# Kernel tuning notes

Hardware: AMD Instinct MI355X
Metric: run time of the kernel (lower is better)

The kernel has to match this reference:

```python
import jax, jax.numpy as jnp
import numpy as np

B, L, D, H = 2, 2048, 1024, 16
P = D // H  # head dim = 64


def setup_inputs() -> dict:
    key = jax.random.key(0)
    ks = jax.random.split(key, 9)
    s = 1.0 / np.sqrt(D)
    x = jax.random.normal(ks[0], (B, L, D), dtype=jnp.float32)
    Wq = jax.random.normal(ks[1], (D, D), dtype=jnp.float32) * s
    bq = jax.random.normal(ks[2], (D,), dtype=jnp.float32) * 0.02
    Wk = jax.random.normal(ks[3], (D, D), dtype=jnp.float32) * s
    bk = jax.random.normal(ks[4], (D,), dtype=jnp.float32) * 0.02
    Wv = jax.random.normal(ks[5], (D, D), dtype=jnp.float32) * s
    bv = jax.random.normal(ks[6], (D,), dtype=jnp.float32) * 0.02
    Wo = jax.random.normal(ks[7], (D, D), dtype=jnp.float32) * s
    bo = jax.random.normal(ks[8], (D,), dtype=jnp.float32) * 0.02
    return {"token_activations": x, "Wq": Wq, "bq": bq, "Wk": Wk, "bk": bk,
            "Wv": Wv, "bv": bv, "Wo": Wo, "bo": bo}


def _split_heads(t):
    # 'b l (h p) -> b h l p'
    b, l, d = t.shape
    return t.reshape(b, l, H, P).transpose(0, 2, 1, 3)


def reference(token_activations, Wq, bq, Wk, bk, Wv, bv, Wo, bo):
    x = token_activations
    q = _split_heads(x @ Wq.T + bq)  # [B,H,L,P]
    k = _split_heads(x @ Wk.T + bk)
    v = _split_heads(x @ Wv.T + bv)
    # pattern[b,h,l,m] = K_l . Q_m / sqrt(P)
    scores = jnp.einsum('bhlp,bhmp->bhlm', k, q) / jnp.sqrt(jnp.float32(P))
    attn = jax.nn.softmax(scores, axis=-2)  # softmax over key axis l
    # out at query position m: sum_l attn[l,m] * V_l
    o = jnp.einsum('bhlm,bhlp->bhmp', attn, v)  # [B,H,L,P] (m indexed)
    o = o.transpose(0, 2, 1, 3).reshape(x.shape[0], x.shape[1], D)  # 'b h m p -> b m (h p)'
    return o @ Wo.T + bo
```

## Files before the change

### kernel.cpp

```cpp
#include <hip/hip_runtime.h>

typedef unsigned short u16;
typedef float f32x4 __attribute__((ext_vector_type(4)));
typedef __bf16 bf16x8 __attribute__((ext_vector_type(8)));
typedef __bf16 bf16x4 __attribute__((ext_vector_type(4)));

#define DEV static __device__ __forceinline__

constexpr int kB = 2;
constexpr int kL = 2048;
constexpr int kD = 1024;
constexpr int kH = 16;
constexpr int kP = 64;
constexpr int kM = kB * kL;
constexpr float kQScale = 0.125f * 1.44269504088896f;

DEV u16 f2bf(float x) {
  union { float f; unsigned u; } v;
  v.f = x;
  unsigned r = v.u + 0x7fffu + ((v.u >> 16) & 1u);
  return (u16)(r >> 16);
}

DEV void gload16(const void* g, void* l) {
  __builtin_amdgcn_global_load_lds(
      (const __attribute__((address_space(1))) unsigned int*)g,
      (__attribute__((address_space(3))) unsigned int*)l, 16, 0, 0);
}

__global__ void cvt_kernel(const float* __restrict__ src, u16* __restrict__ dst, int n4) {
  int i = blockIdx.x * blockDim.x + threadIdx.x;
  if (i >= n4) return;
  float4 v = reinterpret_cast<const float4*>(src)[i];
  uint2 o;
  o.x = (unsigned)f2bf(v.x) | ((unsigned)f2bf(v.y) << 16);
  o.y = (unsigned)f2bf(v.z) | ((unsigned)f2bf(v.w) << 16);
  reinterpret_cast<uint2*>(dst)[i] = o;
}

__global__ void cvtw_kernel(const float* __restrict__ w0, const float* __restrict__ w1,
                            const float* __restrict__ w2, const float* __restrict__ w3,
                            u16* __restrict__ o0, u16* __restrict__ o1,
                            u16* __restrict__ o2, u16* __restrict__ o3) {
  int sel = blockIdx.x >> 10;
  int i = (blockIdx.x & 1023) * 256 + threadIdx.x;
  const float* src = sel == 0 ? w0 : (sel == 1 ? w1 : (sel == 2 ? w2 : w3));
  u16* dst = sel == 0 ? o0 : (sel == 1 ? o1 : (sel == 2 ? o2 : o3));
  float4 v = reinterpret_cast<const float4*>(src)[i];
  uint2 o;
  o.x = (unsigned)f2bf(v.x) | ((unsigned)f2bf(v.y) << 16);
  o.y = (unsigned)f2bf(v.z) | ((unsigned)f2bf(v.w) << 16);
  reinterpret_cast<uint2*>(dst)[i] = o;
}

DEV void gemm_tile(const u16* __restrict__ A, const u16* __restrict__ W,
                   int m0, int n0, u16* As, u16* Bs, f32x4 acc[4][4]) {
  const int tid = threadIdx.x;
  const int w = tid >> 6, lane = tid & 63;
  const int wr = w >> 1, wc = w & 1;
  const int g = lane >> 4, c = lane & 15;
  const int srow = lane >> 2;
  const int skoff = (lane & 3) * 8;

  for (int k0 = 0; k0 < kD; k0 += 32) {
    __syncthreads();
#pragma unroll
    for (int j = 0; j < 2; ++j) {
      const u16* ga = A + (size_t)(m0 + w * 32 + j * 16 + srow) * kD + k0 + skoff;
      gload16(ga, As + (w * 32 + j * 16) * 32);
      const u16* gb = W + (size_t)(n0 + w * 32 + j * 16 + srow) * kD + k0 + skoff;
      gload16(gb, Bs + (w * 32 + j * 16) * 32);
    }
    __syncthreads();

    bf16x8 af[4], bfr[4];
#pragma unroll
    for (int f = 0; f < 4; ++f) {
      af[f]  = *reinterpret_cast<const bf16x8*>(As + (wr * 64 + f * 16 + c) * 32 + g * 8);
      bfr[f] = *reinterpret_cast<const bf16x8*>(Bs + (wc * 64 + f * 16 + c) * 32 + g * 8);
    }
#pragma unroll
    for (int fi = 0; fi < 4; ++fi)
#pragma unroll
      for (int fj = 0; fj < 4; ++fj)
        acc[fi][fj] = __builtin_amdgcn_mfma_f32_16x16x32_bf16(af[fi], bfr[fj], acc[fi][fj], 0, 0, 0);
  }
}

__global__ __launch_bounds__(256) void qkv_kernel(
    const u16* __restrict__ xb,
    const u16* __restrict__ wq, const u16* __restrict__ wk, const u16* __restrict__ wv,
    const float* __restrict__ bq, const float* __restrict__ bk, const float* __restrict__ bv,
    u16* __restrict__ qb, u16* __restrict__ kb, u16* __restrict__ vtb) {
  __shared__ u16 As[128 * 32], Bs[128 * 32];
  const int mb = blockIdx.x, nb = blockIdx.y;
  const int sel = nb >> 3;
  const int m0 = mb * 128, n0 = (nb & 7) * 128;
  const u16* W = sel == 0 ? wq : (sel == 1 ? wk : wv);
  const float* bias = sel == 0 ? bq : (sel == 1 ? bk : bv);

  f32x4 acc[4][4];
#pragma unroll
  for (int i = 0; i < 4; ++i)
#pragma unroll
    for (int j = 0; j < 4; ++j) acc[i][j] = f32x4{0.f, 0.f, 0.f, 0.f};

  gemm_tile(xb, W, m0, n0, As, Bs, acc);

  const int lane = threadIdx.x & 63, w = threadIdx.x >> 6;
  const int wr = w >> 1, wc = w & 1, g = lane >> 4, c = lane & 15;
  u16* dst = sel == 0 ? qb : (sel == 1 ? kb : vtb);
  const bool transposed = (sel == 2);
  const float scale = (sel == 0) ? kQScale : 1.0f;

#pragma unroll
  for (int fj = 0; fj < 4; ++fj) {
    int n = n0 + wc * 64 + fj * 16 + c;
    float bv_ = bias[n];
    int h = n >> 6, p = n & 63;
#pragma unroll
    for (int fi = 0; fi < 4; ++fi) {
#pragma unroll
      for (int r = 0; r < 4; ++r) {
        int m = m0 + wr * 64 + fi * 16 + g * 4 + r;
        int b = m >> 11, l = m & 2047;
        float val = (acc[fi][fj][r] + bv_) * scale;
        size_t idx = transposed
                         ? (((size_t)(b * kH + h)) * kP + p) * kL + l
                         : (((size_t)(b * kH + h)) * kL + l) * kP + p;
        dst[idx] = f2bf(val);
      }
    }
  }
}

__global__ __launch_bounds__(256) void out_kernel(
    const u16* __restrict__ ob, const u16* __restrict__ wo,
    const float* __restrict__ bo, float* __restrict__ out) {
  __shared__ u16 As[128 * 32], Bs[128 * 32];
  const int m0 = blockIdx.x * 128, n0 = blockIdx.y * 128;
  f32x4 acc[4][4];
#pragma unroll
  for (int i = 0; i < 4; ++i)
#pragma unroll
    for (int j = 0; j < 4; ++j) acc[i][j] = f32x4{0.f, 0.f, 0.f, 0.f};

  gemm_tile(ob, wo, m0, n0, As, Bs, acc);

  const int lane = threadIdx.x & 63, w = threadIdx.x >> 6;
  const int wr = w >> 1, wc = w & 1, g = lane >> 4, c = lane & 15;
#pragma unroll
  for (int fj = 0; fj < 4; ++fj) {
    int n = n0 + wc * 64 + fj * 16 + c;
    float bv_ = bo[n];
#pragma unroll
    for (int fi = 0; fi < 4; ++fi) {
#pragma unroll
      for (int r = 0; r < 4; ++r) {
        int m = m0 + wr * 64 + fi * 16 + g * 4 + r;
        out[(size_t)m * kD + n] = acc[fi][fj][r] + bv_;
      }
    }
  }
}

__global__ __launch_bounds__(256, 4) void attn_kernel(
    const u16* __restrict__ qb, const u16* __restrict__ kb,
    const u16* __restrict__ vtb, u16* __restrict__ ob) {
  __shared__ __align__(16) char kvs[2][2][8192];
  __shared__ __align__(16) char pts[4][2048];
  const int tid = threadIdx.x, w = tid >> 6, lane = tid & 63;
  const int g = lane >> 4, c = lane & 15;
  const int h = blockIdx.y, b = blockIdx.z;
  const size_t hoff = ((size_t)(b * kH + h)) * kL * kP;
  const char* Qg = (const char*)(qb + hoff);
  const char* Kg = (const char*)(kb + hoff);
  const char* Vg = (const char*)(vtb + hoff);
  const int q0 = blockIdx.x * 64 + w * 16;

  const int lrow = lane >> 3;
  const int spb = ((lane & 7) ^ lrow) << 4;
  const int r0 = w * 2, r1 = w * 2 + 1;
  const char* kp0 = Kg + (size_t)(r0 * 8 + lrow) * 128 + spb;
  const char* kp1 = Kg + (size_t)(r1 * 8 + lrow) * 128 + spb;
  const char* vp0 = Vg + (size_t)(r0 * 8 + lrow) * (kL * 2) + spb;
  const char* vp1 = Vg + (size_t)(r1 * 8 + lrow) * (kL * 2) + spb;

  auto stage = [&](int buf) {
    gload16(kp0, &kvs[buf][0][r0 * 1024]);
    gload16(kp1, &kvs[buf][0][r1 * 1024]);
    gload16(vp0, &kvs[buf][1][r0 * 1024]);
    gload16(vp1, &kvs[buf][1][r1 * 1024]);
    kp0 += 64 * 128; kp1 += 64 * 128;
    vp0 += 128;      vp1 += 128;
  };

  const int csw = (c & 7) << 4;
  const int kvb0 = c * 128 + ((g * 16) ^ csw);
  const int kvb1 = c * 128 + ((64 + g * 16) ^ csw);
  char* myPt = &pts[w][0];

  bf16x8 qf[2];
#pragma unroll
  for (int kc = 0; kc < 2; ++kc)
    qf[kc] = *reinterpret_cast<const bf16x8*>(Qg + (size_t)(q0 + c) * 128 + kc * 64 + g * 16);

  f32x4 oacc[4];
#pragma unroll
  for (int pt = 0; pt < 4; ++pt) oacc[pt] = f32x4{0.f, 0.f, 0.f, 0.f};
  float Srun = 0.f;

  stage(0);
  __syncthreads();

  constexpr int NT = kL / 64;
  auto body = [&](int cur, int t) {
    if (t + 1 < NT) stage(cur ^ 1);
    const char* Ks = &kvs[cur][0][0];
    const char* Vs = &kvs[cur][1][0];

    f32x4 s[4];
    __builtin_amdgcn_s_setprio(1);
#pragma unroll
    for (int lt = 0; lt < 4; ++lt) {
      bf16x8 k0 = *reinterpret_cast<const bf16x8*>(Ks + lt * 2048 + kvb0);
      bf16x8 k1 = *reinterpret_cast<const bf16x8*>(Ks + lt * 2048 + kvb1);
      f32x4 z = f32x4{0.f, 0.f, 0.f, 0.f};
      z = __builtin_amdgcn_mfma_f32_16x16x32_bf16(k0, qf[0], z, 0, 0, 0);
      z = __builtin_amdgcn_mfma_f32_16x16x32_bf16(k1, qf[1], z, 0, 0, 0);
      s[lt] = z;
    }
    __builtin_amdgcn_s_setprio(0);

    float tsum = 0.f;
#pragma unroll
    for (int lt = 0; lt < 4; ++lt) {
      bf16x4 pv;
#pragma unroll
      for (int r = 0; r < 4; ++r) {
        float p = __builtin_amdgcn_exp2f(s[lt][r]);
        tsum += p;
        pv[r] = (__bf16)p;
      }
      *reinterpret_cast<bf16x4*>(myPt + c * 128 + ((lt * 32 + g * 8) ^ csw)) = pv;
    }
    Srun += tsum;

    bf16x8 pf0 = *reinterpret_cast<const bf16x8*>(myPt + kvb0);
    bf16x8 pf1 = *reinterpret_cast<const bf16x8*>(myPt + kvb1);
    __builtin_amdgcn_s_setprio(1);
#pragma unroll
    for (int pt = 0; pt < 4; ++pt) {
      bf16x8 v0 = *reinterpret_cast<const bf16x8*>(Vs + pt * 2048 + kvb0);
      bf16x8 v1 = *reinterpret_cast<const bf16x8*>(Vs + pt * 2048 + kvb1);
      oacc[pt] = __builtin_amdgcn_mfma_f32_16x16x32_bf16(pf0, v0, oacc[pt], 0, 0, 0);
      oacc[pt] = __builtin_amdgcn_mfma_f32_16x16x32_bf16(pf1, v1, oacc[pt], 0, 0, 0);
    }
    __builtin_amdgcn_s_setprio(0);
    __syncthreads();
  };

  for (int t = 0; t < NT; t += 2) {
    body(0, t);
    body(1, t + 1);
  }

  Srun += __shfl_xor(Srun, 16, 64);
  Srun += __shfl_xor(Srun, 32, 64);

  float rs = 1.f / Srun;
  float fr[4];
#pragma unroll
  for (int r = 0; r < 4; ++r) fr[r] = __shfl(rs, g * 4 + r, 64);
#pragma unroll
  for (int pt = 0; pt < 4; ++pt)
#pragma unroll
    for (int r = 0; r < 4; ++r) {
      int q = q0 + g * 4 + r;
      ob[((size_t)(b * kL + q)) * kD + h * kP + pt * 16 + c] = f2bf(oacc[pt][r] * fr[r]);
    }
}

extern "C" void kernel_launch(void* const* d_in, const int* in_sizes, int n_in,
                              void* d_out, int out_size, void* d_ws, size_t ws_size,
                              hipStream_t stream) {
  (void)in_sizes; (void)n_in; (void)out_size; (void)ws_size;
  const float* x  = (const float*)d_in[0];
  const float* Wq = (const float*)d_in[1];
  const float* bq = (const float*)d_in[2];
  const float* Wk = (const float*)d_in[3];
  const float* bk = (const float*)d_in[4];
  const float* Wv = (const float*)d_in[5];
  const float* bv = (const float*)d_in[6];
  const float* Wo = (const float*)d_in[7];
  const float* bo = (const float*)d_in[8];
  float* out = (float*)d_out;

  char* ws = (char*)d_ws;
  u16* xb  = (u16*)(ws);
  u16* wqb = (u16*)(ws + (8u << 20));
  u16* wkb = (u16*)(ws + (10u << 20));
  u16* wvb = (u16*)(ws + (12u << 20));
  u16* wob = (u16*)(ws + (14u << 20));
  u16* qb  = (u16*)(ws + (16u << 20));
  u16* kb  = (u16*)(ws + (24u << 20));
  u16* vtb = (u16*)(ws + (32u << 20));

  cvt_kernel<<<kM * kD / 1024, 256, 0, stream>>>(x, xb, kM * kD / 4);
  cvtw_kernel<<<4096, 256, 0, stream>>>(Wq, Wk, Wv, Wo, wqb, wkb, wvb, wob);

  qkv_kernel<<<dim3(kM / 128, 24), 256, 0, stream>>>(
      xb, wqb, wkb, wvb, bq, bk, bv, qb, kb, vtb);

  attn_kernel<<<dim3(kL / 64, kH, kB), 256, 0, stream>>>(qb, kb, vtb, xb);

  out_kernel<<<dim3(kM / 128, kD / 128), 256, 0, stream>>>(xb, wob, bo, out);
}
```

Baseline: 124.9 us.

## Double-buffer GEMM tiles, vectorize epilogue stores, widen attention blocks to eight waves

The shared GEMM core now double-buffers the A/B tiles, so the next k-slice loads while MFMAs run on the current one, and it raises wave priority around the MFMA burst. Q/K/out epilogues use swapped MFMA operands, so each lane holds four consecutive columns and can write them as one bf16x4/float4 vector store with a float4 bias load. The V-transposed epilogue writes four consecutive positions per store. The attention kernel moves to 512 threads covering 128 queries per block, so each K/V tile staged in shared memory serves twice as many queries, with fewer loads per wave, at the cost of lower occupancy and larger LDS use.

```diff
diff --git a/kernel.cpp b/kernel.cpp
--- a/kernel.cpp
+++ b/kernel.cpp
@@ -53,7 +53,8 @@
   reinterpret_cast<uint2*>(dst)[i] = o;
 }
 
-DEV void gemm_tile(const u16* __restrict__ A, const u16* __restrict__ W,
+template <bool SWAP>
+DEV void gemm_core(const u16* __restrict__ A, const u16* __restrict__ W,
                    int m0, int n0, u16* As, u16* Bs, f32x4 acc[4][4]) {
   const int tid = threadIdx.x;
   const int w = tid >> 6, lane = tid & 63;
@@ -62,28 +63,54 @@
   const int srow = lane >> 2;
   const int skoff = (lane & 3) * 8;
 
-  for (int k0 = 0; k0 < kD; k0 += 32) {
+  const u16* ga0 = A + (size_t)(m0 + w * 32 + srow) * kD + skoff;
+  const u16* ga1 = ga0 + (size_t)16 * kD;
+  const u16* gb0 = W + (size_t)(n0 + w * 32 + srow) * kD + skoff;
+  const u16* gb1 = gb0 + (size_t)16 * kD;
+  u16* Ad0 = As + (w * 32) * 32;
+  u16* Ad1 = As + (w * 32 + 16) * 32;
+  u16* Bd0 = Bs + (w * 32) * 32;
+  u16* Bd1 = Bs + (w * 32 + 16) * 32;
+
+  auto stage = [&](int buf) {
+    gload16(ga0, Ad0 + buf * 4096);
+    gload16(ga1, Ad1 + buf * 4096);
+    gload16(gb0, Bd0 + buf * 4096);
+    gload16(gb1, Bd1 + buf * 4096);
+    ga0 += 32; ga1 += 32; gb0 += 32; gb1 += 32;
+  };
+
+  auto compute = [&](int buf) {
+    const u16* Ab = As + buf * 4096;
+    const u16* Bb = Bs + buf * 4096;
+    bf16x8 af[4], bfr[4];
+#pragma unroll
+    for (int f = 0; f < 4; ++f) {
+      af[f]  = *reinterpret_cast<const bf16x8*>(Ab + (wr * 64 + f * 16 + c) * 32 + g * 8);
+      bfr[f] = *reinterpret_cast<const bf16x8*>(Bb + (wc * 64 + f * 16 + c) * 32 + g * 8);
+    }
+    __builtin_amdgcn_s_setprio(1);
+#pragma unroll
+    for (int fi = 0; fi < 4; ++fi)
+#pragma unroll
+      for (int fj = 0; fj < 4; ++fj) {
+        if constexpr (SWAP)
+          acc[fj][fi] = __builtin_amdgcn_mfma_f32_16x16x32_bf16(bfr[fj], af[fi], acc[fj][fi], 0, 0, 0);
+        else
+          acc[fi][fj] = __builtin_amdgcn_mfma_f32_16x16x32_bf16(af[fi], bfr[fj], acc[fi][fj], 0, 0, 0);
+      }
+    __builtin_amdgcn_s_setprio(0);
+  };
+
+  stage(0);
+  __syncthreads();
+  for (int k0 = 0; k0 < kD; k0 += 64) {
+    stage(1);
+    compute(0);
     __syncthreads();
-#pragma unroll
-    for (int j = 0; j < 2; ++j) {
-      const u16* ga = A + (size_t)(m0 + w * 32 + j * 16 + srow) * kD + k0 + skoff;
-      gload16(ga, As + (w * 32 + j * 16) * 32);
-      const u16* gb = W + (size_t)(n0 + w * 32 + j * 16 + srow) * kD + k0 + skoff;
-      gload16(gb, Bs + (w * 32 + j * 16) * 32);
-    }
+    if (k0 + 64 < kD) stage(0);
+    compute(1);
     __syncthreads();
-
-    bf16x8 af[4], bfr[4];
-#pragma unroll
-    for (int f = 0; f < 4; ++f) {
-      af[f]  = *reinterpret_cast<const bf16x8*>(As + (wr * 64 + f * 16 + c) * 32 + g * 8);
-      bfr[f] = *reinterpret_cast<const bf16x8*>(Bs + (wc * 64 + f * 16 + c) * 32 + g * 8);
-    }
-#pragma unroll
-    for (int fi = 0; fi < 4; ++fi)
-#pragma unroll
-      for (int fj = 0; fj < 4; ++fj)
-        acc[fi][fj] = __builtin_amdgcn_mfma_f32_16x16x32_bf16(af[fi], bfr[fj], acc[fi][fj], 0, 0, 0);
   }
 }
 
@@ -92,43 +119,60 @@
     const u16* __restrict__ wq, const u16* __restrict__ wk, const u16* __restrict__ wv,
     const float* __restrict__ bq, const float* __restrict__ bk, const float* __restrict__ bv,
     u16* __restrict__ qb, u16* __restrict__ kb, u16* __restrict__ vtb) {
-  __shared__ u16 As[128 * 32], Bs[128 * 32];
+  __shared__ u16 As[2 * 128 * 32], Bs[2 * 128 * 32];
   const int mb = blockIdx.x, nb = blockIdx.y;
   const int sel = nb >> 3;
   const int m0 = mb * 128, n0 = (nb & 7) * 128;
   const u16* W = sel == 0 ? wq : (sel == 1 ? wk : wv);
   const float* bias = sel == 0 ? bq : (sel == 1 ? bk : bv);
 
-  f32x4 acc[4][4];
-#pragma unroll
-  for (int i = 0; i < 4; ++i)
-#pragma unroll
-    for (int j = 0; j < 4; ++j) acc[i][j] = f32x4{0.f, 0.f, 0.f, 0.f};
-
-  gemm_tile(xb, W, m0, n0, As, Bs, acc);
-
   const int lane = threadIdx.x & 63, w = threadIdx.x >> 6;
   const int wr = w >> 1, wc = w & 1, g = lane >> 4, c = lane & 15;
-  u16* dst = sel == 0 ? qb : (sel == 1 ? kb : vtb);
-  const bool transposed = (sel == 2);
-  const float scale = (sel == 0) ? kQScale : 1.0f;
-
-#pragma unroll
-  for (int fj = 0; fj < 4; ++fj) {
-    int n = n0 + wc * 64 + fj * 16 + c;
-    float bv_ = bias[n];
-    int h = n >> 6, p = n & 63;
-#pragma unroll
-    for (int fi = 0; fi < 4; ++fi) {
-#pragma unroll
-      for (int r = 0; r < 4; ++r) {
-        int m = m0 + wr * 64 + fi * 16 + g * 4 + r;
-        int b = m >> 11, l = m & 2047;
-        float val = (acc[fi][fj][r] + bv_) * scale;
-        size_t idx = transposed
-                         ? (((size_t)(b * kH + h)) * kP + p) * kL + l
-                         : (((size_t)(b * kH + h)) * kL + l) * kP + p;
-        dst[idx] = f2bf(val);
+  const int bb = m0 >> 11;
+  const int lbase = (m0 & 2047) + wr * 64;
+
+  f32x4 acc[4][4];
+#pragma unroll
+  for (int i = 0; i < 4; ++i)
+#pragma unroll
+    for (int j = 0; j < 4; ++j) acc[i][j] = f32x4{0.f, 0.f, 0.f, 0.f};
+
+  if (sel < 2) {
+    gemm_core<true>(xb, W, m0, n0, As, Bs, acc);
+    u16* dst = sel == 0 ? qb : kb;
+    const float scale = (sel == 0) ? kQScale : 1.0f;
+#pragma unroll
+    for (int fj = 0; fj < 4; ++fj) {
+      const int n4 = n0 + wc * 64 + fj * 16 + g * 4;
+      const float4 b4 = *reinterpret_cast<const float4*>(&bias[n4]);
+      const int hh = n4 >> 6, p0 = n4 & 63;
+      u16* base = dst + ((size_t)(bb * kH + hh)) * kL * kP + p0;
+#pragma unroll
+      for (int fi = 0; fi < 4; ++fi) {
+        const int l = lbase + fi * 16 + c;
+        bf16x4 o;
+        o[0] = (__bf16)((acc[fj][fi][0] + b4.x) * scale);
+        o[1] = (__bf16)((acc[fj][fi][1] + b4.y) * scale);
+        o[2] = (__bf16)((acc[fj][fi][2] + b4.z) * scale);
+        o[3] = (__bf16)((acc[fj][fi][3] + b4.w) * scale);
+        *reinterpret_cast<bf16x4*>(base + (size_t)l * kP) = o;
+      }
+    }
+  } else {
+    gemm_core<false>(xb, W, m0, n0, As, Bs, acc);
+#pragma unroll
+    for (int fj = 0; fj < 4; ++fj) {
+      const int n = n0 + wc * 64 + fj * 16 + c;
+      const float bv_ = bias[n];
+      const int hh = n >> 6, p = n & 63;
+      u16* base = vtb + (((size_t)(bb * kH + hh)) * kP + p) * kL;
+#pragma unroll
+      for (int fi = 0; fi < 4; ++fi) {
+        const int l4 = lbase + fi * 16 + g * 4;
+        bf16x4 o;
+#pragma unroll
+        for (int r = 0; r < 4; ++r) o[r] = (__bf16)(acc[fi][fj][r] + bv_);
+        *reinterpret_cast<bf16x4*>(base + l4) = o;
       }
     }
   }
@@ -137,7 +181,7 @@
 __global__ __launch_bounds__(256) void out_kernel(
     const u16* __restrict__ ob, const u16* __restrict__ wo,
     const float* __restrict__ bo, float* __restrict__ out) {
-  __shared__ u16 As[128 * 32], Bs[128 * 32];
+  __shared__ u16 As[2 * 128 * 32], Bs[2 * 128 * 32];
   const int m0 = blockIdx.x * 128, n0 = blockIdx.y * 128;
   f32x4 acc[4][4];
 #pragma unroll
@@ -145,30 +189,32 @@
 #pragma unroll
     for (int j = 0; j < 4; ++j) acc[i][j] = f32x4{0.f, 0.f, 0.f, 0.f};
 
-  gemm_tile(ob, wo, m0, n0, As, Bs, acc);
+  gemm_core<true>(ob, wo, m0, n0, As, Bs, acc);
 
   const int lane = threadIdx.x & 63, w = threadIdx.x >> 6;
   const int wr = w >> 1, wc = w & 1, g = lane >> 4, c = lane & 15;
 #pragma unroll
   for (int fj = 0; fj < 4; ++fj) {
-    int n = n0 + wc * 64 + fj * 16 + c;
-    float bv_ = bo[n];
+    const int n4 = n0 + wc * 64 + fj * 16 + g * 4;
+    const float4 b4 = *reinterpret_cast<const float4*>(&bo[n4]);
 #pragma unroll
     for (int fi = 0; fi < 4; ++fi) {
-#pragma unroll
-      for (int r = 0; r < 4; ++r) {
-        int m = m0 + wr * 64 + fi * 16 + g * 4 + r;
-        out[(size_t)m * kD + n] = acc[fi][fj][r] + bv_;
-      }
+      const int m = m0 + wr * 64 + fi * 16 + c;
+      float4 o;
+      o.x = acc[fj][fi][0] + b4.x;
+      o.y = acc[fj][fi][1] + b4.y;
+      o.z = acc[fj][fi][2] + b4.z;
+      o.w = acc[fj][fi][3] + b4.w;
+      *reinterpret_cast<float4*>(&out[(size_t)m * kD + n4]) = o;
     }
   }
 }
 
-__global__ __launch_bounds__(256, 4) void attn_kernel(
+__global__ __launch_bounds__(512, 2) void attn_kernel(
     const u16* __restrict__ qb, const u16* __restrict__ kb,
     const u16* __restrict__ vtb, u16* __restrict__ ob) {
   __shared__ __align__(16) char kvs[2][2][8192];
-  __shared__ __align__(16) char pts[4][2048];
+  __shared__ __align__(16) char pts[8][2048];
   const int tid = threadIdx.x, w = tid >> 6, lane = tid & 63;
   const int g = lane >> 4, c = lane & 15;
   const int h = blockIdx.y, b = blockIdx.z;
@@ -176,23 +222,18 @@
   const char* Qg = (const char*)(qb + hoff);
   const char* Kg = (const char*)(kb + hoff);
   const char* Vg = (const char*)(vtb + hoff);
-  const int q0 = blockIdx.x * 64 + w * 16;
+  const int q0 = blockIdx.x * 128 + w * 16;
 
   const int lrow = lane >> 3;
   const int spb = ((lane & 7) ^ lrow) << 4;
-  const int r0 = w * 2, r1 = w * 2 + 1;
-  const char* kp0 = Kg + (size_t)(r0 * 8 + lrow) * 128 + spb;
-  const char* kp1 = Kg + (size_t)(r1 * 8 + lrow) * 128 + spb;
-  const char* vp0 = Vg + (size_t)(r0 * 8 + lrow) * (kL * 2) + spb;
-  const char* vp1 = Vg + (size_t)(r1 * 8 + lrow) * (kL * 2) + spb;
+  const char* kp = Kg + (size_t)(w * 8 + lrow) * 128 + spb;
+  const char* vp = Vg + (size_t)(w * 8 + lrow) * (kL * 2) + spb;
 
   auto stage = [&](int buf) {
-    gload16(kp0, &kvs[buf][0][r0 * 1024]);
-    gload16(kp1, &kvs[buf][0][r1 * 1024]);
-    gload16(vp0, &kvs[buf][1][r0 * 1024]);
-    gload16(vp1, &kvs[buf][1][r1 * 1024]);
-    kp0 += 64 * 128; kp1 += 64 * 128;
-    vp0 += 128;      vp1 += 128;
+    gload16(kp, &kvs[buf][0][w * 1024]);
+    gload16(vp, &kvs[buf][1][w * 1024]);
+    kp += 64 * 128;
+    vp += 128;
   };
 
   const int csw = (c & 7) << 4;
@@ -312,7 +353,7 @@
   qkv_kernel<<<dim3(kM / 128, 24), 256, 0, stream>>>(
       xb, wqb, wkb, wvb, bq, bk, bv, qb, kb, vtb);
 
-  attn_kernel<<<dim3(kL / 64, kH, kB), 256, 0, stream>>>(qb, kb, vtb, xb);
+  attn_kernel<<<dim3(kL / 128, kH, kB), 512, 0, stream>>>(qb, kb, vtb, xb);
 
   out_kernel<<<dim3(kM / 128, kD / 128), 256, 0, stream>>>(xb, wob, bo, out);
 }
```

Result: slower. 134.1 us (+7.4%).
